# Kernel tuning notes

Measured on AMD Instinct MI355X. Metric: run time of the kernel, lower is better.

Reference implementation:

```python
import jax, jax.numpy as jnp
import numpy as np

U, L, B = 512, 512, 256  # units, num_layers (rectangular mesh: L == U), batch
PI = float(np.pi)


def cc_mul(a, b):
    # complex multiply of stacked (real, imag) tensors
    return jnp.stack((a[0] * b[0] - a[1] * b[1], a[0] * b[1] + a[1] * b[0]))


def i_mul(c):
    # s_mul(1j, c): multiply stacked complex by 1j -> (-im, re)
    return jnp.stack((-c[1], c[0]))


def setup_inputs() -> dict:
    key = jax.random.key(0)
    ks = jax.random.split(key, 8)
    x = jax.random.normal(ks[0], (2, B, U), jnp.float32)
    two_pi = 2.0 * PI
    theta = jax.random.uniform(ks[1], (L, U // 2), jnp.float32) * two_pi
    phi = jax.random.uniform(ks[2], (L, U // 2), jnp.float32) * two_pi
    gamma = jax.random.uniform(ks[3], (U,), jnp.float32) * two_pi
    mask = jnp.ones((L, U // 2), jnp.float32)
    enn = jax.random.uniform(ks[4], (U, L), jnp.float32)
    enp = jax.random.uniform(ks[5], (U, L), jnp.float32)
    epn = jax.random.uniform(ks[6], (U, L), jnp.float32)
    epp = jax.random.uniform(ks[7], (U, L), jnp.float32)
    # rectangular-mesh permutations: identity at input/output, interior layers
    # alternate circular shifts so MZIs couple (0,1),(2,3),... then (1,2),(3,4),...
    perms = np.tile(np.arange(U, dtype=np.int32), (L + 1, 1))
    for l in range(1, L):
        perms[l] = np.roll(perms[l], 1 if l % 2 else -1)
    perms = jnp.asarray(perms)
    # pairwise off-diagonal permutation: swap adjacent pairs [1,0,3,2,...]
    pairwise_perm = jnp.asarray(
        np.arange(U, dtype=np.int32).reshape(-1, 2)[:, ::-1].ravel())
    return dict(x=x, theta=theta, phi=phi, gamma=gamma, mask=mask,
                enn=enn, enp=enp, epn=epn, epp=epp,
                perms=perms, pairwise_perm=pairwise_perm)


def reference(x, theta, phi, gamma, mask, enn, enp, epn, epp, perms, pairwise_perm):
    # --- MeshPhasesTorch (basis='sm', hadamard=False) ---
    inv = 1.0 - mask
    th = theta * mask + inv * PI  # (1 - hadamard) * pi
    ph = phi * mask + inv * PI

    def stripe(p):  # single_mode_arrangement: [L, U//2] -> [U, L]
        return jnp.zeros((U, L), p.dtype).at[::2].set(p.T)

    internal = stripe(th)
    external = stripe(ph)
    ipsl = jnp.stack((jnp.cos(internal), jnp.sin(internal)))  # [2, U, L]
    epsl = jnp.stack((jnp.cos(external), jnp.sin(external)))  # [2, U, L]

    roll_m1 = lambda t: jnp.roll(t, -1, axis=1)  # along units axis
    roll_p1 = lambda t: jnp.roll(t, 1, axis=1)

    # --- MeshTorch.mesh_layers (hadamard=False branch) ---
    s11 = epp * ipsl - enn * roll_m1(ipsl)
    s22 = roll_p1(-enn * ipsl + epp * roll_m1(ipsl))
    s12 = i_mul(roll_p1(enp * ipsl + epn * roll_m1(ipsl)))
    s21 = i_mul(epn * ipsl + enp * roll_m1(ipsl))

    diag = cc_mul(epsl, s11 + s22) * 0.5              # [2, U, L]
    off = cc_mul(roll_p1(epsl), s21 + s12) * 0.5      # [2, U, L]
    diag = jnp.transpose(diag, (0, 2, 1))             # [2, L, U]
    off = jnp.transpose(off, (0, 2, 1))

    # --- forward: input phase shift, then sequential vertical layers ---
    in_ps = jnp.stack((jnp.cos(gamma), jnp.sin(gamma)))  # [2, U]
    out = cc_mul(x, in_ps[:, None, :])                   # [2, B, U]
    out = out[..., perms[0]]                             # left perm of layer 0

    def step(carry, inp):
        d, o, rp = inp  # [2, U], [2, U], [U]
        y = cc_mul(carry, d[:, None, :]) \
            + cc_mul(carry, o[:, None, :])[..., pairwise_perm]
        return y[..., rp], None

    xs = (jnp.moveaxis(diag, 1, 0), jnp.moveaxis(off, 1, 0), perms[1:])
    out, _ = jax.lax.scan(step, out, xs)
    return out
```

## Files before the change

### kernel.cpp

```cpp
#include <hip/hip_runtime.h>
#include <hip/hip_fp16.h>


#define UU 512
#define LL 512
#define BB 256
#define KK 256
#define KF 4
#define N9 128
#define W9 9
#define N17 64
#define W17 17
#define N33 32
#define W33 33


__global__ __launch_bounds__(512, 2) void mesh_build4(
    const float* __restrict__ theta, const float* __restrict__ phi,
    const float* __restrict__ enn,   const float* __restrict__ enp,
    const float* __restrict__ epn,   const float* __restrict__ epp,
    float2* __restrict__ g9)
{
    __shared__ float2 gwj[7 * UU];
    __shared__ float2 xbuf[2][UU];
    const int u  = threadIdx.x;
    const int j  = ((blockIdx.x & 7) << 4) | (blockIdx.x >> 3);
    const int um = (u + UU - 1) & (UU - 1);
    const int l0 = j * KF;

    const float4 epp_u4 = *(const float4*)(epp + u * LL + l0);
    const float4 epp_m4 = *(const float4*)(epp + um * LL + l0);
    const float4 enn_u4 = *(const float4*)(enn + u * LL + l0);
    const float4 enn_m4 = *(const float4*)(enn + um * LL + l0);
    const float4 enp_u4 = *(const float4*)(enp + u * LL + l0);
    const float4 enp_m4 = *(const float4*)(enp + um * LL + l0);
    const float4 epn_u4 = *(const float4*)(epn + u * LL + l0);
    const float4 epn_m4 = *(const float4*)(epn + um * LL + l0);
    const float epp_u8[4] = {epp_u4.x, epp_u4.y, epp_u4.z, epp_u4.w};
    const float epp_m8[4] = {epp_m4.x, epp_m4.y, epp_m4.z, epp_m4.w};
    const float enn_u8[4] = {enn_u4.x, enn_u4.y, enn_u4.z, enn_u4.w};
    const float enn_m8[4] = {enn_m4.x, enn_m4.y, enn_m4.z, enn_m4.w};
    const float enp_u8[4] = {enp_u4.x, enp_u4.y, enp_u4.z, enp_u4.w};
    const float enp_m8[4] = {enp_m4.x, enp_m4.y, enp_m4.z, enp_m4.w};
    const float epn_u8[4] = {epn_u4.x, epn_u4.y, epn_u4.z, epn_u4.w};
    const float epn_m8[4] = {epn_m4.x, epn_m4.y, epn_m4.z, epn_m4.w};

    const int ka = u >> 1;
    const int kb = ((u + 1) >> 1) & (KK - 1);
    float thA[KF], thB[KF], phC[KF];
    #pragma unroll
    for (int s = 0; s < KF; ++s) {
        thA[s] = theta[(l0 + s) * KK + ka];
        thB[s] = theta[(l0 + s) * KK + kb];
        phC[s] = phi  [(l0 + s) * KK + ka];
    }

    const bool uodd = (u & 1) != 0;

    #define COEF(s, DR, DI, OR_, OI_) { \
        float sA, cA, sB, cB, sC, cC; \
        __sincosf(thA[s], &sA, &cA); \
        __sincosf(thB[s], &sB, &cB); \
        __sincosf(phC[s], &sC, &cC); \
        const float ipu_r = uodd ? 1.f : cA, ipu_i = uodd ? 0.f : sA; \
        const float ipp_r = uodd ? cB : 1.f, ipp_i = uodd ? sB : 0.f; \
        const float ipm_r = uodd ? cA : 1.f, ipm_i = uodd ? sA : 0.f; \
        const float epu_r = uodd ? 1.f : cC, epu_i = uodd ? 0.f : sC; \
        const float epm_r = uodd ? cC : 1.f, epm_i = uodd ? sC : 0.f; \
        const float sd_r = epp_u8[s]*ipu_r - enn_u8[s]*ipp_r - enn_m8[s]*ipm_r + epp_m8[s]*ipu_r; \
        const float sd_i = epp_u8[s]*ipu_i - enn_u8[s]*ipp_i - enn_m8[s]*ipm_i + epp_m8[s]*ipu_i; \
        DR = 0.5f * (epu_r * sd_r - epu_i * sd_i); \
        DI = 0.5f * (epu_r * sd_i + epu_i * sd_r); \
        const float so_r = epn_u8[s]*ipu_r + enp_u8[s]*ipp_r + enp_m8[s]*ipm_r + epn_m8[s]*ipu_r; \
        const float so_i = epn_u8[s]*ipu_i + enp_u8[s]*ipp_i + enp_m8[s]*ipm_i + epn_m8[s]*ipu_i; \
        const float soi_r = -so_i, soi_i = so_r; \
        OR_ = 0.5f * (epm_r * soi_r - epm_i * soi_i); \
        OI_ = 0.5f * (epm_r * soi_i + epm_i * soi_r); }

    float dcur_r, dcur_i, o0_r, o0_i;
    COEF(0, dcur_r, dcur_i, o0_r, o0_i)
    gwj[u] = make_float2(1.f, 0.f);
    xbuf[0][u] = make_float2(o0_r, o0_i);
    __syncthreads();

    int sigma = 0;
    const int tb = uodd ? 0 : 2;
    float2 outr[W9];

    #pragma unroll
    for (int s = 0; s < KF; ++s) {
        const int W  = 2 * s + 1;
        const int Wn = W + 2;
        const int a  = (u + sigma) & (UU - 1);
        const int bx = ((u ^ 1) + sigma) & (UU - 1);
        const float2 ox = xbuf[s & 1][u ^ 1];
        const float dr = dcur_r, di = dcur_i, orr = ox.x, oi = ox.y;

        #pragma unroll
        for (int tn = 0; tn < W9; ++tn) {
            float ar = 0.f, ai = 0.f;
            if (tn < Wn) {
                const int tp = tn - 1;
                const int ts = tn - tb;
                if (0 <= tp && tp < W) {
                    float2 gv = gwj[tp * UU + a];
                    ar += dr * gv.x - di * gv.y;
                    ai += dr * gv.y + di * gv.x;
                }
                if (0 <= ts && ts < W) {
                    float2 gv = gwj[ts * UU + bx];
                    ar += orr * gv.x - oi * gv.y;
                    ai += orr * gv.y + oi * gv.x;
                }
            }
            outr[tn] = make_float2(ar, ai);
        }

        if (s < KF - 1) {
            float dn_r, dn_i, on_r, on_i;
            COEF(s + 1, dn_r, dn_i, on_r, on_i)
            __syncthreads();
            const int wd = (u + sigma) & (UU - 1);
            #pragma unroll
            for (int tn = 0; tn < W9; ++tn)
                if (tn < Wn) gwj[tn * UU + wd] = outr[tn];
            xbuf[(s + 1) & 1][u] = make_float2(on_r, on_i);
            dcur_r = dn_r; dcur_i = dn_i;
            sigma += (s & 1) ? 1 : -1;
            __syncthreads();
        }
    }
    #undef COEF

    const int v = (j == N9 - 1) ? u : um;
    #pragma unroll
    for (int t = 0; t < W9; ++t)
        g9[(j * W9 + t) * UU + v] = outr[t];
}

__global__ __launch_bounds__(512, 2) void mesh_merge_both(
    const float2* __restrict__ g9, __half2* __restrict__ g2h)
{
    __shared__ float2 lds1[W17 * UU];
    const int u = threadIdx.x;
    const int q = blockIdx.x;

    {
        const int jA = 4 * q + 1, jB = 4 * q;
        float2 a[W9];
        #pragma unroll
        for (int ta = 0; ta < W9; ++ta)
            a[ta] = g9[(jA * W9 + ta) * UU + u];

        float2 outv[W17];
        #pragma unroll
        for (int t = 0; t < W17; ++t) outv[t] = make_float2(0.f, 0.f);

        #pragma unroll
        for (int ta = 0; ta < W9; ++ta) {
            const int k = (u - 4 + ta + UU) & (UU - 1);
            float2 brow[W9];
            #pragma unroll
            for (int tbq = 0; tbq < W9; ++tbq)
                brow[tbq] = g9[(jB * W9 + tbq) * UU + k];
            #pragma unroll
            for (int tbq = 0; tbq < W9; ++tbq) {
                outv[ta + tbq].x += a[ta].x * brow[tbq].x - a[ta].y * brow[tbq].y;
                outv[ta + tbq].y += a[ta].x * brow[tbq].y + a[ta].y * brow[tbq].x;
            }
        }
        #pragma unroll
        for (int t = 0; t < W17; ++t) lds1[t * UU + u] = outv[t];
    }

    float2 r2[W17];
    {
        const int jA = 4 * q + 3, jB = 4 * q + 2;
        const int loA = (jA == N9 - 1) ? -5 : -4;
        float2 a[W9];
        #pragma unroll
        for (int ta = 0; ta < W9; ++ta)
            a[ta] = g9[(jA * W9 + ta) * UU + u];

        #pragma unroll
        for (int t = 0; t < W17; ++t) r2[t] = make_float2(0.f, 0.f);

        #pragma unroll
        for (int ta = 0; ta < W9; ++ta) {
            const int k = (u + loA + ta + UU) & (UU - 1);
            float2 brow[W9];
            #pragma unroll
            for (int tbq = 0; tbq < W9; ++tbq)
                brow[tbq] = g9[(jB * W9 + tbq) * UU + k];
            #pragma unroll
            for (int tbq = 0; tbq < W9; ++tbq) {
                r2[ta + tbq].x += a[ta].x * brow[tbq].x - a[ta].y * brow[tbq].y;
                r2[ta + tbq].y += a[ta].x * brow[tbq].y + a[ta].y * brow[tbq].x;
            }
        }
    }
    __syncthreads();

    {
        const int loC = (q == N33 - 1) ? -9 : -8;
        float2 outv[W33];
        #pragma unroll
        for (int t = 0; t < W33; ++t) outv[t] = make_float2(0.f, 0.f);

        #pragma unroll
        for (int ta = 0; ta < W17; ++ta) {
            const int k = (u + loC + ta + UU) & (UU - 1);
            #pragma unroll
            for (int tbq = 0; tbq < W17; ++tbq) {
                const float2 bv = lds1[tbq * UU + k];
                outv[ta + tbq].x += r2[ta].x * bv.x - r2[ta].y * bv.y;
                outv[ta + tbq].y += r2[ta].x * bv.y + r2[ta].y * bv.x;
            }
        }
        #pragma unroll
        for (int t = 0; t < W33; ++t)
            g2h[(q * W33 + t) * UU + u] = __floats2half2_rn(outv[t].x, outv[t].y);
    }
}

__global__ __launch_bounds__(512, 2) void mesh_apply(
    const float* __restrict__ x, const float* __restrict__ gamma,
    const __half2* __restrict__ g2h, float* __restrict__ out)
{
    __shared__ float2 sbuf[2][548];
    const int u = threadIdx.x;
    const int b = blockIdx.x;

    float sg, cg;
    __sincosf(gamma[u], &sg, &cg);
    const float xr = x[b * UU + u];
    const float xi = x[BB * UU + b * UU + u];
    float2 v = make_float2(xr * cg - xi * sg, xr * sg + xi * cg);

    #define STORE_STATE(pp)                                                   \
        do {                                                                  \
            sbuf[pp][u + 17] = v;                                             \
            if (u >= 495) sbuf[pp][u - 495] = v;          \
            if (u < 16)   sbuf[pp][u + 529] = v;          \
        } while (0)

    STORE_STATE(0);

    float2 gg[W33];
    {
        const __half2* gq = g2h + u;
        #pragma unroll
        for (int t = 0; t < W33; ++t) gg[t] = __half22float2(gq[t * UU]);
    }
    __syncthreads();

    for (int q = 0; q < N33; ++q) {
        const int p = q & 1;
        const int base = u + ((q == N33 - 1) ? 0 : 1);

        float2 w[W33];
        #pragma unroll
        for (int t = 0; t < W33; ++t) w[t] = sbuf[p][base + t];

        float ar = 0.f, ai = 0.f;
        #pragma unroll
        for (int t = 0; t < W33; ++t) {
            ar += gg[t].x * w[t].x - gg[t].y * w[t].y;
            ai += gg[t].x * w[t].y + gg[t].y * w[t].x;
        }
        v = make_float2(ar, ai);

        if (q < N33 - 1) {
            const __half2* gq = g2h + (q + 1) * (W33 * UU) + u;
            #pragma unroll
            for (int t = 0; t < W33; ++t) gg[t] = __half22float2(gq[t * UU]);
            STORE_STATE(1 - p);
            __syncthreads();
        }
    }

    out[b * UU + u]           = v.x;
    out[BB * UU + b * UU + u] = v.y;
    #undef STORE_STATE
}

#define RSLOTS 6
#define WAITVM40() __builtin_amdgcn_s_waitcnt(0x8F78)
#define STAGE(gg, ss)                                                        \
    _Pragma("unroll")                                                        \
    for (int jq = 0; jq < 8; ++jq)                                           \
        __builtin_amdgcn_global_load_lds(                                    \
            (const __attribute__((address_space(1))) void*)(coef + (gg) * UU + jq * 64 + lane), \
            (__attribute__((address_space(3))) void*)&ring[(ss) * UU + jq * 64], \
            16, 0, 0);

__global__ __launch_bounds__(512) void mesh_precompute_slot(
    const float* __restrict__ theta, const float* __restrict__ phi,
    const float* __restrict__ enn,   const float* __restrict__ enp,
    const float* __restrict__ epn,   const float* __restrict__ epp,
    float4* __restrict__ coef)
{
    const int u  = threadIdx.x;
    const int l  = blockIdx.x;
    const int um = (u + UU - 1) & (UU - 1);
    const float epp_u  = epp[u * LL + l],  epp_um = epp[um * LL + l];
    const float enn_u  = enn[u * LL + l],  enn_um = enn[um * LL + l];
    const float enp_u  = enp[u * LL + l],  enp_um = enp[um * LL + l];
    const float epn_u  = epn[u * LL + l],  epn_um = epn[um * LL + l];
    float ipu_r, ipu_i, ipp_r, ipp_i, ipm_r, ipm_i;
    float epu_r, epu_i, epm_r, epm_i;
    if ((u & 1) == 0) {
        const int k = u >> 1;
        float th = theta[l * KK + k];  __sincosf(th, &ipu_i, &ipu_r);
        ipp_r = 1.f; ipp_i = 0.f;  ipm_r = 1.f; ipm_i = 0.f;
        float phv = phi[l * KK + k];   __sincosf(phv, &epu_i, &epu_r);
        epm_r = 1.f; epm_i = 0.f;
    } else {
        ipu_r = 1.f; ipu_i = 0.f;
        float thp = theta[l * KK + (((u + 1) >> 1) & (KK - 1))]; __sincosf(thp, &ipp_i, &ipp_r);
        float thm = theta[l * KK + (u >> 1)];                    __sincosf(thm, &ipm_i, &ipm_r);
        epu_r = 1.f; epu_i = 0.f;
        float phm = phi[l * KK + (u >> 1)];                      __sincosf(phm, &epm_i, &epm_r);
    }
    const float sd_r = epp_u * ipu_r - enn_u * ipp_r - enn_um * ipm_r + epp_um * ipu_r;
    const float sd_i = epp_u * ipu_i - enn_u * ipp_i - enn_um * ipm_i + epp_um * ipu_i;
    const float d_r = 0.5f * (epu_r * sd_r - epu_i * sd_i);
    const float d_i = 0.5f * (epu_r * sd_i + epu_i * sd_r);
    const float so_r = epn_u * ipu_r + enp_u * ipp_r + enp_um * ipm_r + epn_um * ipu_r;
    const float so_i = epn_u * ipu_i + enp_u * ipp_i + enp_um * ipm_i + epn_um * ipu_i;
    const float soi_r = -so_i, soi_i = so_r;
    const float o_r = 0.5f * (epm_r * soi_r - epm_i * soi_i);
    const float o_i = 0.5f * (epm_r * soi_i + epm_i * soi_r);
    const int slot = ((u & 7) << 6) | (u >> 3);
    coef[l * UU + slot] = make_float4(d_r, d_i, o_r, o_i);
}

#define PAIR_MIX(K)                                                         \
    _Pragma("unroll")                                                       \
    for (int p = 0; p < 4; ++p) {                                           \
        const float4 ke = K[2*p], ko = K[2*p+1];                            \
        y0r[p] = c0r[p]*ke.x - c0i[p]*ke.y + c1r[p]*ko.z - c1i[p]*ko.w;     \
        y0i[p] = c0r[p]*ke.y + c0i[p]*ke.x + c1r[p]*ko.w + c1i[p]*ko.z;     \
        y1r[p] = c1r[p]*ko.x - c1i[p]*ko.y + c0r[p]*ke.z - c0i[p]*ke.w;     \
        y1i[p] = c1r[p]*ko.y + c1i[p]*ko.x + c0r[p]*ke.w + c0i[p]*ke.z;     \
    }

__global__ __launch_bounds__(64) void mesh_chain_r3(
    const float* __restrict__ x, const float* __restrict__ gamma,
    const float4* __restrict__ coef, float* __restrict__ out)
{
    __shared__ float4 ring[RSLOTS * UU];
    const int lane = threadIdx.x;
    const int b    = blockIdx.x;
    const int m0   = lane << 3;
    #pragma unroll
    for (int pl = 0; pl < RSLOTS; ++pl) { STAGE(pl, pl) }
    const float4 xr0 = *(const float4*)(x + b * UU + m0);
    const float4 xr1 = *(const float4*)(x + b * UU + m0 + 4);
    const float4 xi0 = *(const float4*)(x + BB * UU + b * UU + m0);
    const float4 xi1 = *(const float4*)(x + BB * UU + b * UU + m0 + 4);
    const float xr[8] = {xr0.x, xr0.y, xr0.z, xr0.w, xr1.x, xr1.y, xr1.z, xr1.w};
    const float xi[8] = {xi0.x, xi0.y, xi0.z, xi0.w, xi1.x, xi1.y, xi1.z, xi1.w};
    float c0r[4], c0i[4], c1r[4], c1i[4];
    #pragma unroll
    for (int p = 0; p < 4; ++p) {
        float s0, cg0, s1, cg1;
        __sincosf(gamma[m0 + 2*p],     &s0, &cg0);
        __sincosf(gamma[m0 + 2*p + 1], &s1, &cg1);
        c0r[p] = xr[2*p] * cg0 - xi[2*p] * s0;
        c0i[p] = xr[2*p] * s0  + xi[2*p] * cg0;
        c1r[p] = xr[2*p+1] * cg1 - xi[2*p+1] * s1;
        c1i[p] = xr[2*p+1] * s1  + xi[2*p+1] * cg1;
    }
    const int laneM1 = (lane + 63) & 63;
    const int laneP1 = (lane + 1) & 63;
    int sa = 0;
    for (int it = 0; it < 256; ++it) {
        float y0r[4], y0i[4], y1r[4], y1i[4];
        WAITVM40();
        float4 k[8];
        #pragma unroll
        for (int q = 0; q < 8; ++q) k[q] = ring[sa * UU + q * 64 + lane];
        PAIR_MIX(k)
        {
            const float br = __shfl(y1r[3], laneM1, 64);
            const float bi = __shfl(y1i[3], laneM1, 64);
            #pragma unroll
            for (int p = 3; p > 0; --p) { c0r[p] = y1r[p-1]; c0i[p] = y1i[p-1]; }
            c0r[0] = br; c0i[0] = bi;
            #pragma unroll
            for (int p = 0; p < 4; ++p) { c1r[p] = y0r[p]; c1i[p] = y0i[p]; }
        }
        { const int g1 = (2 * it + RSLOTS) & (LL - 1); STAGE(g1, sa) }
        WAITVM40();
        float4 n[8];
        #pragma unroll
        for (int q = 0; q < 8; ++q) n[q] = ring[(sa + 1) * UU + q * 64 + lane];
        PAIR_MIX(n)
        if (it < 255) {
            const float br = __shfl(y0r[0], laneP1, 64);
            const float bi = __shfl(y0i[0], laneP1, 64);
            #pragma unroll
            for (int p = 0; p < 3; ++p) { c0r[p] = y1r[p]; c0i[p] = y1i[p];
                                          c1r[p] = y0r[p+1]; c1i[p] = y0i[p+1]; }
            c0r[3] = y1r[3]; c0i[3] = y1i[3];
            c1r[3] = br;     c1i[3] = bi;
        } else {
            #pragma unroll
            for (int p = 0; p < 4; ++p) { c0r[p] = y0r[p]; c0i[p] = y0i[p];
                                          c1r[p] = y1r[p]; c1i[p] = y1i[p]; }
        }
        { const int g2 = (2 * it + RSLOTS + 1) & (LL - 1); STAGE(g2, sa + 1) }
        sa += 2; if (sa >= RSLOTS) sa = 0;
    }
    *(float4*)(out + b * UU + m0)               = make_float4(c0r[0], c1r[0], c0r[1], c1r[1]);
    *(float4*)(out + b * UU + m0 + 4)           = make_float4(c0r[2], c1r[2], c0r[3], c1r[3]);
    *(float4*)(out + BB * UU + b * UU + m0)     = make_float4(c0i[0], c1i[0], c0i[1], c1i[1]);
    *(float4*)(out + BB * UU + b * UU + m0 + 4) = make_float4(c0i[2], c1i[2], c0i[3], c1i[3]);
}

extern "C" void kernel_launch(void* const* d_in, const int* in_sizes, int n_in,
                              void* d_out, int out_size, void* d_ws, size_t ws_size,
                              hipStream_t stream) {
    (void)in_sizes; (void)n_in; (void)out_size;
    const float* x     = (const float*)d_in[0];
    const float* theta = (const float*)d_in[1];
    const float* phi   = (const float*)d_in[2];
    const float* gamma = (const float*)d_in[3];
    const float* enn   = (const float*)d_in[5];
    const float* enp   = (const float*)d_in[6];
    const float* epn   = (const float*)d_in[7];
    const float* epp   = (const float*)d_in[8];
    float* out = (float*)d_out;

    if (ws_size >= (size_t)6881280) {
        float2*  g9  = (float2*)d_ws;
        __half2* g2h = (__half2*)((char*)d_ws + 4718592);

        mesh_build4<<<N9, UU, 0, stream>>>(theta, phi, enn, enp, epn, epp, g9);
        mesh_merge_both<<<N33, UU, 0, stream>>>(g9, g2h);
        mesh_apply<<<BB, UU, 0, stream>>>(x, gamma, g2h, out);
    } else {
        float4* coef = (float4*)d_ws;
        mesh_precompute_slot<<<LL, UU, 0, stream>>>(theta, phi, enn, enp, epn, epp, coef);
        mesh_chain_r3<<<BB, 64, 0, stream>>>(x, gamma, coef, out);
    }
}
```

Measured before the change: 151.5 us.

## Split banded-matrix merge across column chunks to raise block count

The merge kernel that combines four 9-wide banded factors into one 33-wide banded factor now runs as 256 blocks instead of 32, with each block handling a 64-column chunk. Each output element is computed by its own thread, and halo columns for the first product are kept in shared memory. This addresses the low occupancy of the old 32-block launch, which left most compute units idle and held large per-thread register arrays. The cost is redundant recomputation of the 16 halo columns in each chunk and more global reads of the factor data.

```diff
diff --git a/kernel.cpp b/kernel.cpp
--- a/kernel.cpp
+++ b/kernel.cpp
@@ -138,88 +138,76 @@
         g9[(j * W9 + t) * UU + v] = outr[t];
 }
 
-__global__ __launch_bounds__(512, 2) void mesh_merge_both(
+__global__ __launch_bounds__(512, 2) void mesh_merge33(
     const float2* __restrict__ g9, __half2* __restrict__ g2h)
 {
-    __shared__ float2 lds1[W17 * UU];
-    const int u = threadIdx.x;
-    const int q = blockIdx.x;
-
-    {
-        const int jA = 4 * q + 1, jB = 4 * q;
-        float2 a[W9];
-        #pragma unroll
-        for (int ta = 0; ta < W9; ++ta)
-            a[ta] = g9[(jA * W9 + ta) * UU + u];
-
-        float2 outv[W17];
-        #pragma unroll
-        for (int t = 0; t < W17; ++t) outv[t] = make_float2(0.f, 0.f);
-
-        #pragma unroll
-        for (int ta = 0; ta < W9; ++ta) {
-            const int k = (u - 4 + ta + UU) & (UU - 1);
-            float2 brow[W9];
-            #pragma unroll
-            for (int tbq = 0; tbq < W9; ++tbq)
-                brow[tbq] = g9[(jB * W9 + tbq) * UU + k];
-            #pragma unroll
-            for (int tbq = 0; tbq < W9; ++tbq) {
-                outv[ta + tbq].x += a[ta].x * brow[tbq].x - a[ta].y * brow[tbq].y;
-                outv[ta + tbq].y += a[ta].x * brow[tbq].y + a[ta].y * brow[tbq].x;
+    __shared__ float2 A1[W17 * 80];
+    __shared__ float2 A2[W17 * 64];
+    const int tid = threadIdx.x;
+    const int q   = blockIdx.x & 31;
+    const int c   = blockIdx.x >> 5;
+    const int u0  = c << 6;
+    const int loA2  = (q == N33 - 1) ? -5 : -4;
+    const int loC   = (q == N33 - 1) ? -9 : -8;
+    const int kbase = u0 + loC;
+
+    const float2* __restrict__ g9a = g9 + (4 * q    ) * W9 * UU;
+    const float2* __restrict__ g9b = g9 + (4 * q + 1) * W9 * UU;
+    const float2* __restrict__ g9c = g9 + (4 * q + 2) * W9 * UU;
+    const float2* __restrict__ g9d = g9 + (4 * q + 3) * W9 * UU;
+
+    for (int e = tid; e < W17 * 80; e += 512) {
+        const int tb = e / 80;
+        const int kk = e - tb * 80;
+        const int k  = (kbase + kk + UU) & (UU - 1);
+        float ar = 0.f, ai = 0.f;
+        #pragma unroll
+        for (int a = 0; a < W9; ++a) {
+            const int tbm = tb - a;
+            if (0 <= tbm && tbm < W9) {
+                const float2 va = g9b[a * UU + k];
+                const float2 vb = g9a[tbm * UU + ((k - 4 + a + UU) & (UU - 1))];
+                ar += va.x * vb.x - va.y * vb.y;
+                ai += va.x * vb.y + va.y * vb.x;
             }
         }
-        #pragma unroll
-        for (int t = 0; t < W17; ++t) lds1[t * UU + u] = outv[t];
-    }
-
-    float2 r2[W17];
-    {
-        const int jA = 4 * q + 3, jB = 4 * q + 2;
-        const int loA = (jA == N9 - 1) ? -5 : -4;
-        float2 a[W9];
-        #pragma unroll
-        for (int ta = 0; ta < W9; ++ta)
-            a[ta] = g9[(jA * W9 + ta) * UU + u];
-
-        #pragma unroll
-        for (int t = 0; t < W17; ++t) r2[t] = make_float2(0.f, 0.f);
-
-        #pragma unroll
-        for (int ta = 0; ta < W9; ++ta) {
-            const int k = (u + loA + ta + UU) & (UU - 1);
-            float2 brow[W9];
-            #pragma unroll
-            for (int tbq = 0; tbq < W9; ++tbq)
-                brow[tbq] = g9[(jB * W9 + tbq) * UU + k];
-            #pragma unroll
-            for (int tbq = 0; tbq < W9; ++tbq) {
-                r2[ta + tbq].x += a[ta].x * brow[tbq].x - a[ta].y * brow[tbq].y;
-                r2[ta + tbq].y += a[ta].x * brow[tbq].y + a[ta].y * brow[tbq].x;
+        A1[e] = make_float2(ar, ai);
+    }
+
+    for (int e = tid; e < W17 * 64; e += 512) {
+        const int ta = e >> 6;
+        const int uu = e & 63;
+        const int u  = u0 + uu;
+        float ar = 0.f, ai = 0.f;
+        #pragma unroll
+        for (int a = 0; a < W9; ++a) {
+            const int tam = ta - a;
+            if (0 <= tam && tam < W9) {
+                const float2 va = g9d[a * UU + u];
+                const float2 vb = g9c[tam * UU + ((u + loA2 + a + UU) & (UU - 1))];
+                ar += va.x * vb.x - va.y * vb.y;
+                ai += va.x * vb.y + va.y * vb.x;
             }
         }
+        A2[e] = make_float2(ar, ai);
     }
     __syncthreads();
 
-    {
-        const int loC = (q == N33 - 1) ? -9 : -8;
-        float2 outv[W33];
-        #pragma unroll
-        for (int t = 0; t < W33; ++t) outv[t] = make_float2(0.f, 0.f);
-
+    for (int e = tid; e < W33 * 64; e += 512) {
+        const int t  = e >> 6;
+        const int uu = e & 63;
+        float ar = 0.f, ai = 0.f;
         #pragma unroll
         for (int ta = 0; ta < W17; ++ta) {
-            const int k = (u + loC + ta + UU) & (UU - 1);
-            #pragma unroll
-            for (int tbq = 0; tbq < W17; ++tbq) {
-                const float2 bv = lds1[tbq * UU + k];
-                outv[ta + tbq].x += r2[ta].x * bv.x - r2[ta].y * bv.y;
-                outv[ta + tbq].y += r2[ta].x * bv.y + r2[ta].y * bv.x;
+            const int tbm = t - ta;
+            if (0 <= tbm && tbm < W17) {
+                const float2 va = A2[ta * 64 + uu];
+                const float2 vb = A1[tbm * 80 + uu + ta];
+                ar += va.x * vb.x - va.y * vb.y;
+                ai += va.x * vb.y + va.y * vb.x;
             }
         }
-        #pragma unroll
-        for (int t = 0; t < W33; ++t)
-            g2h[(q * W33 + t) * UU + u] = __floats2half2_rn(outv[t].x, outv[t].y);
+        g2h[(q * W33 + t) * UU + (u0 + uu)] = __floats2half2_rn(ar, ai);
     }
 }
 
@@ -438,7 +426,7 @@
         __half2* g2h = (__half2*)((char*)d_ws + 4718592);
 
         mesh_build4<<<N9, UU, 0, stream>>>(theta, phi, enn, enp, epn, epp, g9);
-        mesh_merge_both<<<N33, UU, 0, stream>>>(g9, g2h);
+        mesh_merge33<<<N33 * 8, UU, 0, stream>>>(g9, g2h);
         mesh_apply<<<BB, UU, 0, stream>>>(x, gamma, g2h, out);
     } else {
         float4* coef = (float4*)d_ws;
```

After: 144.3 us. 4.8% less time.
